# Performance work log

Hardware: AMD Instinct MI355X
Metric: run time of the kernel (lower is better)

Reference implementation:

```python
import jax, jax.numpy as jnp
import numpy as np

NUM_LAYERS = 2
D = 1024          # d_model
H = 16            # nhead
HD = D // H       # head_dim = 64
FF = 4096         # dim_feedforward
S, N, L = 1024, 2, 4096
EPS = 1e-5


def _layer_norm(x, g, b):
    mu = jnp.mean(x, axis=-1, keepdims=True)
    var = jnp.var(x, axis=-1, keepdims=True)
    return (x - mu) * jax.lax.rsqrt(var + EPS) * g + b


def setup_inputs() -> dict:
    key = jax.random.key(0)
    ks = jax.random.split(key, 16)
    w = 0.02
    return {
        "key_in": jax.random.normal(ks[0], (S, N, D), jnp.float32),
        "value_in": jax.random.normal(ks[1], (S, N, D), jnp.float32),
        "query": jax.random.normal(ks[2], (L, N, D), jnp.float32),
        "in_proj_w": jax.random.normal(ks[3], (NUM_LAYERS, 3 * D, D), jnp.float32) * w,
        "in_proj_b": jnp.zeros((NUM_LAYERS, 3 * D), jnp.float32),
        "out_w": jax.random.normal(ks[4], (NUM_LAYERS, D, D), jnp.float32) * w,
        "out_b": jnp.zeros((NUM_LAYERS, D), jnp.float32),
        "ln1_g": jnp.ones((NUM_LAYERS, D), jnp.float32),
        "ln1_b": jnp.zeros((NUM_LAYERS, D), jnp.float32),
        "ln2_g": jnp.ones((NUM_LAYERS, D), jnp.float32),
        "ln2_b": jnp.zeros((NUM_LAYERS, D), jnp.float32),
        "ff1_w": jax.random.normal(ks[5], (NUM_LAYERS, FF, D), jnp.float32) * w,
        "ff1_b": jnp.zeros((NUM_LAYERS, FF), jnp.float32),
        "ff2_w": jax.random.normal(ks[6], (NUM_LAYERS, D, FF), jnp.float32) * w,
        "ff2_b": jnp.zeros((NUM_LAYERS, D), jnp.float32),
    }


def reference(key_in, value_in, query, in_proj_w, in_proj_b, out_w, out_b,
              ln1_g, ln1_b, ln2_g, ln2_b, ff1_w, ff1_b, ff2_w, ff2_b):
    scaling = float(HD) ** -0.5
    noise_key = jax.random.key(42)
    tgt = query
    attn_map = None
    for i in range(NUM_LAYERS):
        Wq, Wk, Wv = in_proj_w[i, :D], in_proj_w[i, D:2 * D], in_proj_w[i, 2 * D:]
        bq, bk, bv = in_proj_b[i, :D], in_proj_b[i, D:2 * D], in_proj_b[i, 2 * D:]
        q = (tgt @ Wq.T + bq) * scaling              # [L,N,D]
        k = key_in @ Wk.T + bk                       # [S,N,D]
        v = value_in @ Wv.T + bv                     # [S,N,D]
        qh = q.reshape(L, N, H, HD).transpose(1, 2, 0, 3)   # [N,H,L,HD]
        kh = k.reshape(S, N, H, HD).transpose(1, 2, 0, 3)   # [N,H,S,HD]
        vh = v.reshape(S, N, H, HD).transpose(1, 2, 0, 3)   # [N,H,S,HD]
        scores = jnp.einsum('nhld,nhsd->nhls', qh, kh)      # [N,H,L,S]
        # add_noise_term: zero logit column + random value token
        scores = jnp.concatenate(
            [scores, jnp.zeros((N, H, L, 1), scores.dtype)], axis=-1)
        noise = jax.random.normal(jax.random.fold_in(noise_key, i),
                                  (N, H, 1, HD), vh.dtype)
        vh = jnp.concatenate([vh, noise], axis=2)           # [N,H,S+1,HD]
        w = jax.nn.softmax(scores, axis=-1)                 # [N,H,L,S+1]
        seg = jax.nn.sigmoid(w)                             # sigmoid of softmax
        out = jnp.einsum('nhls,nhsd->nhld', w, vh)          # [N,H,L,HD]
        out = out.transpose(2, 0, 1, 3).reshape(L, N, D)
        out = out @ out_w[i].T + out_b[i]
        attn_map = seg.mean(axis=1)[:, :, :-1]              # [N,L,S], noise col dropped
        x = _layer_norm(tgt + out, ln1_g[i], ln1_b[i])
        h = jax.nn.relu(x @ ff1_w[i].T + ff1_b[i]) @ ff2_w[i].T + ff2_b[i]
        tgt = _layer_norm(x + h, ln2_g[i], ln2_b[i])
    return tgt, attn_map
```

## Files before the change

### kernel.cpp

```cpp
#include <hip/hip_runtime.h>
#include <hip/hip_bf16.h>


typedef __bf16 bf16x8 __attribute__((ext_vector_type(8)));
typedef float  f32x4  __attribute__((ext_vector_type(4)));

__device__ __forceinline__ f32x4 mfma16(bf16x8 a, bf16x8 b, f32x4 c) {
    return __builtin_amdgcn_mfma_f32_16x16x32_bf16(a, b, c, 0, 0, 0);
}

__device__ __forceinline__ void load_lds16(const __bf16* g, __bf16* l) {
    __builtin_amdgcn_global_load_lds(
        (const __attribute__((address_space(1))) void*)g,
        (__attribute__((address_space(3))) void*)l, 16, 0, 0);
}

__device__ __forceinline__ int swz8(int o, int nwg) {
    return (o & 7) * (nwg >> 3) + (o >> 3);
}

__global__ __launch_bounds__(256) void cast_k(const float* __restrict__ in,
                                              __bf16* __restrict__ out, int n4) {
    int i = blockIdx.x * 256 + threadIdx.x;
    if (i >= n4) return;
    float4 f = ((const float4*)in)[i];
    union { uint2 u; __bf16 h[4]; } ob;
    ob.h[0] = (__bf16)f.x; ob.h[1] = (__bf16)f.y;
    ob.h[2] = (__bf16)f.z; ob.h[3] = (__bf16)f.w;
    ((uint2*)out)[i] = ob.u;
}

__global__ __launch_bounds__(512, 2) void gemm8p(
    const __bf16* __restrict__ A, const __bf16* __restrict__ B,
    const float* __restrict__ bias, __bf16* __restrict__ C,
    int Mt, int N, int K, float scale, int relu)
{
    __shared__ __bf16 L[8][8192];
    const int tid = threadIdx.x;
    const int wid = tid >> 6, lane = tid & 63;
    const int lq = lane >> 4, lc = lane & 15;
    const int wm = wid >> 2;
    const int wn = (wid & 3) * 64;
    const int bh = wn >> 7;
    const int lb = wn & 127;
    const int sw = lc & 7;
    const int w = swz8(blockIdx.x, gridDim.x);
    const int bm = (w % Mt) * 256, bn = (w / Mt) * 256;
    const int NT = K >> 6;

    auto stageA = [&](int kt, int h) {
#pragma unroll
        for (int p = 0; p < 2; ++p) {
            const int cc = p * 512 + tid;
            const int row = cc >> 3, gk = ((cc & 7) ^ (row & 7)) * 8;
            load_lds16(A + (size_t)(bm + h * 128 + row) * K + (kt * 64 + gk),
                       &L[(kt & 1) * 4 + h][(size_t)cc * 8]);
        }
    };
    auto stageB = [&](int kt, int h) {
#pragma unroll
        for (int p = 0; p < 2; ++p) {
            const int cc = p * 512 + tid;
            const int row = cc >> 3, gk = ((cc & 7) ^ (row & 7)) * 8;
            load_lds16(B + (size_t)(bn + h * 128 + row) * K + (kt * 64 + gk),
                       &L[(kt & 1) * 4 + 2 + h][(size_t)cc * 8]);
        }
    };

    stageA(0, 0); stageA(0, 1); stageB(0, 0); stageB(0, 1);
    stageA(1, 0); stageA(1, 1); stageB(1, 0); stageB(1, 1);
    asm volatile("s_waitcnt vmcnt(8)" ::: "memory");
    __builtin_amdgcn_s_barrier();
    __builtin_amdgcn_sched_barrier(0);

    const f32x4 fz = {0.f, 0.f, 0.f, 0.f};
    f32x4 acc[2][4][4];
#pragma unroll
    for (int rh = 0; rh < 2; ++rh)
#pragma unroll
        for (int i = 0; i < 4; ++i)
#pragma unroll
            for (int jj = 0; jj < 4; ++jj) acc[rh][i][jj] = fz;

    for (int t = 0; t < NT; ++t) {
        const __bf16* __restrict__ Ah = &L[(t & 1) * 4 + wm][0];
        const __bf16* __restrict__ Bh = &L[(t & 1) * 4 + 2 + bh][0];
        const int pf = (t + 2 < NT);
        bf16x8 a[2][4], b0[2][2], b1[2][2];

#pragma unroll
        for (int kk = 0; kk < 2; ++kk) {
            const int sl = ((kk * 4 + lq) ^ sw) * 8;
#pragma unroll
            for (int i = 0; i < 4; ++i)
                a[kk][i] = *(const bf16x8*)&Ah[(i * 16 + lc) * 64 + sl];
#pragma unroll
            for (int j = 0; j < 2; ++j)
                b0[kk][j] = *(const bf16x8*)&Bh[(lb + j * 16 + lc) * 64 + sl];
        }
        __builtin_amdgcn_s_barrier();
        asm volatile("s_waitcnt lgkmcnt(0)" ::: "memory");
        __builtin_amdgcn_sched_barrier(0);
        __builtin_amdgcn_s_setprio(1);
#pragma unroll
        for (int kk = 0; kk < 2; ++kk)
#pragma unroll
            for (int i = 0; i < 4; ++i)
#pragma unroll
                for (int j = 0; j < 2; ++j)
                    acc[0][i][j] = mfma16(a[kk][i], b0[kk][j], acc[0][i][j]);
        __builtin_amdgcn_s_setprio(0);
        __builtin_amdgcn_s_barrier();
        __builtin_amdgcn_sched_barrier(0);

#pragma unroll
        for (int kk = 0; kk < 2; ++kk) {
            const int sl = ((kk * 4 + lq) ^ sw) * 8;
#pragma unroll
            for (int j = 0; j < 2; ++j)
                b1[kk][j] = *(const bf16x8*)&Bh[(lb + 32 + j * 16 + lc) * 64 + sl];
        }
        __builtin_amdgcn_s_barrier();
        asm volatile("s_waitcnt lgkmcnt(0)" ::: "memory");
        __builtin_amdgcn_sched_barrier(0);
        __builtin_amdgcn_s_setprio(1);
#pragma unroll
        for (int kk = 0; kk < 2; ++kk)
#pragma unroll
            for (int i = 0; i < 4; ++i)
#pragma unroll
                for (int j = 0; j < 2; ++j)
                    acc[0][i][2 + j] = mfma16(a[kk][i], b1[kk][j], acc[0][i][2 + j]);
        __builtin_amdgcn_s_setprio(0);
        __builtin_amdgcn_s_barrier();
        __builtin_amdgcn_sched_barrier(0);

#pragma unroll
        for (int kk = 0; kk < 2; ++kk) {
            const int sl = ((kk * 4 + lq) ^ sw) * 8;
#pragma unroll
            for (int i = 0; i < 4; ++i)
                a[kk][i] = *(const bf16x8*)&Ah[(64 + i * 16 + lc) * 64 + sl];
        }
        if (pf) { stageB(t + 2, 0); stageB(t + 2, 1); }
        __builtin_amdgcn_s_barrier();
        asm volatile("s_waitcnt lgkmcnt(0)" ::: "memory");
        __builtin_amdgcn_sched_barrier(0);
        __builtin_amdgcn_s_setprio(1);
#pragma unroll
        for (int kk = 0; kk < 2; ++kk)
#pragma unroll
            for (int i = 0; i < 4; ++i)
#pragma unroll
                for (int j = 0; j < 2; ++j)
                    acc[1][i][j] = mfma16(a[kk][i], b0[kk][j], acc[1][i][j]);
        __builtin_amdgcn_s_setprio(0);
        __builtin_amdgcn_s_barrier();
        __builtin_amdgcn_sched_barrier(0);

        if (pf) { stageA(t + 2, 0); stageA(t + 2, 1); }
        __builtin_amdgcn_s_barrier();
        __builtin_amdgcn_sched_barrier(0);
        __builtin_amdgcn_s_setprio(1);
#pragma unroll
        for (int kk = 0; kk < 2; ++kk)
#pragma unroll
            for (int i = 0; i < 4; ++i)
#pragma unroll
                for (int j = 0; j < 2; ++j)
                    acc[1][i][2 + j] = mfma16(a[kk][i], b1[kk][j], acc[1][i][2 + j]);
        __builtin_amdgcn_s_setprio(0);
        if (pf) asm volatile("s_waitcnt vmcnt(8)" ::: "memory");
        else    asm volatile("s_waitcnt vmcnt(0)" ::: "memory");
        __builtin_amdgcn_s_barrier();
        __builtin_amdgcn_sched_barrier(0);
    }

    float bv[4];
#pragma unroll
    for (int q = 0; q < 4; ++q) bv[q] = bias[bn + wn + q * 16 + lc];
#pragma unroll
    for (int rh = 0; rh < 2; ++rh)
#pragma unroll
        for (int i = 0; i < 4; ++i)
#pragma unroll
            for (int r = 0; r < 4; ++r) {
                const int row = bm + wm * 128 + rh * 64 + i * 16 + lq * 4 + r;
                const size_t base = (size_t)row * N + bn + wn + lc;
#pragma unroll
                for (int ch = 0; ch < 2; ++ch)
#pragma unroll
                    for (int j = 0; j < 2; ++j) {
                        float v = (acc[rh][i][ch * 2 + j][r] + bv[ch * 2 + j]) * scale;
                        if (relu) v = fmaxf(v, 0.f);
                        C[base + ch * 32 + j * 16] = (__bf16)v;
                    }
            }
}

template <int BN>
__device__ __forceinline__ void gemm_core(
    const __bf16* __restrict__ A, const __bf16* __restrict__ B,
    const float* __restrict__ bias, __bf16* __restrict__ C,
    int M, int N, int K, float scale, int relu, int bm, int bn,
    __bf16* As, __bf16* Bs)
{
    const int tid = threadIdx.x;
    const int wave = tid >> 6, lane = tid & 63;
    const int lq = lane >> 4, lc = lane & 15;
    const int WN = BN / 2;
    const int JT = WN / 16;
    const int wm = (wave >> 1) * 64, wn = (wave & 1) * WN;

    const f32x4 fz = {0.f, 0.f, 0.f, 0.f};
    f32x4 acc[4][4];
#pragma unroll
    for (int i = 0; i < 4; ++i)
#pragma unroll
        for (int j = 0; j < JT; ++j) acc[i][j] = fz;

    const int sw = lc & 7;

    for (int k0 = 0; k0 < K; k0 += 64) {
        __syncthreads();
#pragma unroll
        for (int i = 0; i < 4; ++i) {
            const int c = tid + 256 * i;
            const int row = c >> 3, gk = ((c & 7) ^ (row & 7)) * 8;
            load_lds16(A + (size_t)(bm + row) * K + (k0 + gk),
                       As + (size_t)c * 8);
        }
#pragma unroll
        for (int i = 0; i < BN / 32; ++i) {
            const int c = tid + 256 * i;
            const int row = c >> 3, gk = ((c & 7) ^ (row & 7)) * 8;
            load_lds16(B + (size_t)(bn + row) * K + (k0 + gk),
                       Bs + (size_t)c * 8);
        }
        __syncthreads();
#pragma unroll
        for (int kk = 0; kk < 2; ++kk) {
            bf16x8 af[4], bw[4];
            const int slot = ((kk * 4 + lq) ^ sw) * 8;
#pragma unroll
            for (int i = 0; i < 4; ++i)
                af[i] = *(const bf16x8*)&As[(wm + i * 16 + lc) * 64 + slot];
#pragma unroll
            for (int j = 0; j < JT; ++j)
                bw[j] = *(const bf16x8*)&Bs[(wn + j * 16 + lc) * 64 + slot];
#pragma unroll
            for (int i = 0; i < 4; ++i)
#pragma unroll
                for (int j = 0; j < JT; ++j)
                    acc[i][j] = mfma16(af[i], bw[j], acc[i][j]);
        }
    }

#pragma unroll
    for (int j = 0; j < JT; ++j) {
        const int col = bn + wn + j * 16 + lc;
        const float bv = bias[col];
#pragma unroll
        for (int i = 0; i < 4; ++i) {
#pragma unroll
            for (int r = 0; r < 4; ++r) {
                float v = (acc[i][j][r] + bv) * scale;
                if (relu) v = fmaxf(v, 0.f);
                const int row = bm + wm + i * 16 + lq * 4 + r;
                C[(size_t)row * N + col] = (__bf16)v;
            }
        }
    }
}

__global__ __launch_bounds__(256) void gemm64(
    const __bf16* __restrict__ A, const __bf16* __restrict__ B,
    const float* __restrict__ bias, __bf16* __restrict__ C,
    int M, int N, int K, float scale, int relu)
{
    __shared__ __bf16 As[128 * 64];
    __shared__ __bf16 Bs[64 * 64];
    const int nwg = gridDim.x * gridDim.y;
    const int o = blockIdx.y * gridDim.x + blockIdx.x;
    const int w = swz8(o, nwg);
    const int bx = w % gridDim.x, by = w / gridDim.x;
    gemm_core<64>(A, B, bias, C, M, N, K, scale, relu,
                  by * 128, bx * 64, As, Bs);
}

__global__ __launch_bounds__(256) void gemm_qkv(
    const __bf16* __restrict__ TGT, const __bf16* __restrict__ KIN,
    const __bf16* __restrict__ VIN, const __bf16* __restrict__ W,
    const float* __restrict__ bias, __bf16* __restrict__ PROJ,
    __bf16* __restrict__ KB, __bf16* __restrict__ VB)
{
    __shared__ __bf16 As[128 * 64];
    __shared__ __bf16 Bs[64 * 64];
    const int bid = swz8(blockIdx.x, 1536);
    const __bf16* A; __bf16* Cout; int M, t, seg; float scale;
    if (bid < 1024)      { seg = 0; t = bid;        A = TGT; Cout = PROJ; M = 8192; scale = 0.125f; }
    else if (bid < 1280) { seg = 1; t = bid - 1024; A = KIN; Cout = KB;   M = 2048; scale = 1.f; }
    else                 { seg = 2; t = bid - 1280; A = VIN; Cout = VB;   M = 2048; scale = 1.f; }
    gemm_core<64>(A, W + (size_t)seg * 1048576, bias + seg * 1024, Cout,
                  M, 1024, 1024, scale, 0, (t >> 4) * 128, (t & 15) * 64, As, Bs);
}

__global__ __launch_bounds__(256) void transpose_v(const __bf16* __restrict__ v,
                                                   __bf16* __restrict__ vt) {
    __shared__ __bf16 t[64][72];
    const int tid = threadIdx.x;
    const int s0 = blockIdx.x * 64, h = blockIdx.y, n = blockIdx.z;
#pragma unroll
    for (int i = 0; i < 2; ++i) {
        const int cc = tid + 256 * i, row = cc >> 3, kc = (cc & 7) * 8;
        *(uint4*)&t[row][kc] =
            *(const uint4*)(v + ((size_t)((s0 + row) * 2 + n)) * 1024 + h * 64 + kc);
    }
    __syncthreads();
#pragma unroll
    for (int i = 0; i < 2; ++i) {
        const int cc = tid + 256 * i, d = cc >> 3, jc = (cc & 7) * 8;
        __attribute__((aligned(16))) __bf16 tmp[8];
#pragma unroll
        for (int u = 0; u < 8; ++u) tmp[u] = t[jc + u][d];
        *(uint4*)(vt + ((size_t)((n * 16 + h) * 64 + d)) * 1024 + s0 + jc) = *(uint4*)tmp;
    }
}

__global__ __launch_bounds__(256) void attn_fused(
    const __bf16* __restrict__ q, const __bf16* __restrict__ kk,
    const __bf16* __restrict__ vt, float* __restrict__ cvec,
    __bf16* __restrict__ aout)
{
    __shared__ __bf16 qs[64][72];
    __shared__ __bf16 ks[64][72];
    __shared__ __bf16 vs[64][72];
    __shared__ __bf16 es[64][72];
    const int tid = threadIdx.x, wave = tid >> 6, lane = tid & 63;
    const int lq = lane >> 4, lc = lane & 15;
    const int o = (blockIdx.z * 16 + blockIdx.y) * 64 + blockIdx.x;
    const int w = swz8(o, 2048);
    const int l0 = (w & 63) * 64, h = (w >> 6) & 15, n = w >> 10;
    const int wr = wave * 16;
#pragma unroll
    for (int i = 0; i < 2; ++i) {
        const int cc = tid + 256 * i, row = cc >> 3, kc = (cc & 7) * 8;
        *(uint4*)&qs[row][kc] =
            *(const uint4*)(q + ((size_t)((l0 + row) * 2 + n)) * 1024 + h * 64 + kc);
    }
    const f32x4 fz = {0.f, 0.f, 0.f, 0.f};
    f32x4 oacc[4];
#pragma unroll
    for (int dj = 0; dj < 4; ++dj) oacc[dj] = fz;
    float den[4] = {0.f, 0.f, 0.f, 0.f};

    for (int st = 0; st < 16; ++st) {
        __syncthreads();
#pragma unroll
        for (int i = 0; i < 2; ++i) {
            const int cc = tid + 256 * i, row = cc >> 3, kc = (cc & 7) * 8;
            *(uint4*)&ks[row][kc] =
                *(const uint4*)(kk + ((size_t)((st * 64 + row) * 2 + n)) * 1024 + h * 64 + kc);
            *(uint4*)&vs[row][kc] =
                *(const uint4*)(vt + ((size_t)((n * 16 + h) * 64 + row)) * 1024 + st * 64 + kc);
        }
        __syncthreads();
        const bf16x8 a0 = *(const bf16x8*)&qs[wr + lc][lq * 8];
        const bf16x8 a1 = *(const bf16x8*)&qs[wr + lc][32 + lq * 8];
#pragma unroll
        for (int sj = 0; sj < 4; ++sj) {
            f32x4 acc = fz;
            const bf16x8 b0 = *(const bf16x8*)&ks[sj * 16 + lc][lq * 8];
            const bf16x8 b1 = *(const bf16x8*)&ks[sj * 16 + lc][32 + lq * 8];
            acc = mfma16(a0, b0, acc);
            acc = mfma16(a1, b1, acc);
#pragma unroll
            for (int r = 0; r < 4; ++r) {
                const float e = __expf(acc[r]);
                den[r] += e;
                es[wr + lq * 4 + r][sj * 16 + lc] = (__bf16)e;
            }
        }
        const bf16x8 w0 = *(const bf16x8*)&es[wr + lc][lq * 8];
        const bf16x8 w1 = *(const bf16x8*)&es[wr + lc][32 + lq * 8];
#pragma unroll
        for (int dj = 0; dj < 4; ++dj) {
            const bf16x8 v0 = *(const bf16x8*)&vs[dj * 16 + lc][lq * 8];
            const bf16x8 v1 = *(const bf16x8*)&vs[dj * 16 + lc][32 + lq * 8];
            oacc[dj] = mfma16(w0, v0, oacc[dj]);
            oacc[dj] = mfma16(w1, v1, oacc[dj]);
        }
    }
#pragma unroll
    for (int m = 1; m < 16; m <<= 1)
#pragma unroll
        for (int r = 0; r < 4; ++r) den[r] += __shfl_xor(den[r], m);
    float c_r[4];
#pragma unroll
    for (int r = 0; r < 4; ++r) c_r[r] = 1.f / (den[r] + 1.f);
    if (lc == 0) {
#pragma unroll
        for (int r = 0; r < 4; ++r)
            cvec[((size_t)(n * 16 + h)) * 4096 + (l0 + wr + lq * 4 + r)] = c_r[r];
    }
#pragma unroll
    for (int r = 0; r < 4; ++r) {
        const int l = l0 + wr + lq * 4 + r;
        const size_t base = ((size_t)l * 2 + n) * 1024 + h * 64 + lc;
#pragma unroll
        for (int dj = 0; dj < 4; ++dj)
            aout[base + dj * 16] = (__bf16)(oacc[dj][r] * c_r[r]);
    }
}

__global__ __launch_bounds__(256) void attn_map_k(
    const __bf16* __restrict__ q, const __bf16* __restrict__ kk,
    const float* __restrict__ cvec, float* __restrict__ amap)
{
    __shared__ __bf16 qs[64][72];
    __shared__ __bf16 ks[64][72];
    const int tid = threadIdx.x, wave = tid >> 6, lane = tid & 63;
    const int lq = lane >> 4, lc = lane & 15;
    const int o = (blockIdx.z * 16 + blockIdx.y) * 64 + blockIdx.x;
    const int w = swz8(o, 2048);
    const int l0 = (w & 63) * 64, st = (w >> 6) & 15, n = w >> 10;
    const int wr = wave * 16;
    float sig[4][4];
#pragma unroll
    for (int sj = 0; sj < 4; ++sj)
#pragma unroll
        for (int r = 0; r < 4; ++r) sig[sj][r] = 0.f;

    for (int h = 0; h < 16; ++h) {
        __syncthreads();
#pragma unroll
        for (int i = 0; i < 2; ++i) {
            const int cc = tid + 256 * i, row = cc >> 3, kc = (cc & 7) * 8;
            *(uint4*)&qs[row][kc] =
                *(const uint4*)(q + ((size_t)((l0 + row) * 2 + n)) * 1024 + h * 64 + kc);
            *(uint4*)&ks[row][kc] =
                *(const uint4*)(kk + ((size_t)((st * 64 + row) * 2 + n)) * 1024 + h * 64 + kc);
        }
        __syncthreads();
        float c_r[4];
#pragma unroll
        for (int r = 0; r < 4; ++r)
            c_r[r] = cvec[((size_t)(n * 16 + h)) * 4096 + (l0 + wr + lq * 4 + r)];
        const bf16x8 a0 = *(const bf16x8*)&qs[wr + lc][lq * 8];
        const bf16x8 a1 = *(const bf16x8*)&qs[wr + lc][32 + lq * 8];
#pragma unroll
        for (int sj = 0; sj < 4; ++sj) {
            const f32x4 fz = {0.f, 0.f, 0.f, 0.f};
            f32x4 acc = fz;
            const bf16x8 b0 = *(const bf16x8*)&ks[sj * 16 + lc][lq * 8];
            const bf16x8 b1 = *(const bf16x8*)&ks[sj * 16 + lc][32 + lq * 8];
            acc = mfma16(a0, b0, acc);
            acc = mfma16(a1, b1, acc);
#pragma unroll
            for (int r = 0; r < 4; ++r) {
                const float ww = __expf(acc[r]) * c_r[r];
                const float w2 = ww * ww;
                sig[sj][r] += 0.5f + ww * (0.25f - w2 * (1.f / 48.f - w2 * (1.f / 480.f)));
            }
        }
    }
#pragma unroll
    for (int r = 0; r < 4; ++r) {
        const int l = l0 + wr + lq * 4 + r;
        const size_t base = ((size_t)n * 4096 + l) * 1024 + st * 64 + lc;
#pragma unroll
        for (int sj = 0; sj < 4; ++sj)
            amap[base + sj * 16] = sig[sj][r] * (1.f / 16.f);
    }
}

__global__ __launch_bounds__(256) void ln_k(
    const float* __restrict__ basef, const __bf16* __restrict__ baseb,
    const __bf16* __restrict__ add,
    const float* __restrict__ g, const float* __restrict__ bb,
    float* __restrict__ out_f32, __bf16* __restrict__ out_bf)
{
    __shared__ float red[8];
    const int row = blockIdx.x, tid = threadIdx.x;
    const int col = tid * 4;
    const size_t off = (size_t)row * 1024 + col;
    float v[4];
    if (basef) {
        float4 t = *(const float4*)(basef + off);
        v[0] = t.x; v[1] = t.y; v[2] = t.z; v[3] = t.w;
    } else {
        union { uint2 u; __bf16 h[4]; } tb;
        tb.u = *(const uint2*)(baseb + off);
#pragma unroll
        for (int j = 0; j < 4; ++j) v[j] = (float)tb.h[j];
    }
    {
        union { uint2 u; __bf16 h[4]; } ub;
        ub.u = *(const uint2*)(add + off);
#pragma unroll
        for (int j = 0; j < 4; ++j) v[j] += (float)ub.h[j];
    }
    float s = v[0] + v[1] + v[2] + v[3];
    float q = v[0] * v[0] + v[1] * v[1] + v[2] * v[2] + v[3] * v[3];
#pragma unroll
    for (int m = 1; m < 64; m <<= 1) { s += __shfl_xor(s, m); q += __shfl_xor(q, m); }
    const int wave = tid >> 6, lane = tid & 63;
    if (lane == 0) { red[wave] = s; red[4 + wave] = q; }
    __syncthreads();
    s = red[0] + red[1] + red[2] + red[3];
    q = red[4] + red[5] + red[6] + red[7];
    const float mu = s * (1.f / 1024.f);
    const float var = q * (1.f / 1024.f) - mu * mu;
    const float rs = rsqrtf(var + 1e-5f);
    const float4 gv = *(const float4*)(g + col);
    const float4 bv = *(const float4*)(bb + col);
    float y[4];
    y[0] = (v[0] - mu) * rs * gv.x + bv.x;
    y[1] = (v[1] - mu) * rs * gv.y + bv.y;
    y[2] = (v[2] - mu) * rs * gv.z + bv.z;
    y[3] = (v[3] - mu) * rs * gv.w + bv.w;
    if (out_f32) {
        float4 o; o.x = y[0]; o.y = y[1]; o.z = y[2]; o.w = y[3];
        *(float4*)(out_f32 + off) = o;
    }
    if (out_bf) {
        union { uint2 u; __bf16 h[4]; } ob;
#pragma unroll
        for (int j = 0; j < 4; ++j) ob.h[j] = (__bf16)y[j];
        *(uint2*)(out_bf + off) = ob.u;
    }
}

extern "C" void kernel_launch(void* const* d_in, const int* in_sizes, int n_in,
                              void* d_out, int out_size, void* d_ws, size_t ws_size,
                              hipStream_t stream) {
    const float* key_in    = (const float*)d_in[0];
    const float* value_in  = (const float*)d_in[1];
    const float* query     = (const float*)d_in[2];
    const float* in_proj_w = (const float*)d_in[3];
    const float* in_proj_b = (const float*)d_in[4];
    const float* out_w     = (const float*)d_in[5];
    const float* out_b     = (const float*)d_in[6];
    const float* ln1_g     = (const float*)d_in[7];
    const float* ln1_b     = (const float*)d_in[8];
    const float* ln2_g     = (const float*)d_in[9];
    const float* ln2_b     = (const float*)d_in[10];
    const float* ff1_w     = (const float*)d_in[11];
    const float* ff1_b     = (const float*)d_in[12];
    const float* ff2_w     = (const float*)d_in[13];
    const float* ff2_b     = (const float*)d_in[14];
    float* outp = (float*)d_out;

    __bf16* ws = (__bf16*)d_ws;
    const size_t M1 = 1048576;
    __bf16* WQKV = ws;
    __bf16* WOUT = ws + 6 * M1;
    __bf16* WF1  = ws + 8 * M1;
    __bf16* WF2  = ws + 16 * M1;
    __bf16* KIN  = ws + 24 * M1;
    __bf16* VIN  = ws + 26 * M1;
    __bf16* TGT  = ws + 28 * M1;
    __bf16* PROJ = ws + 36 * M1;
    __bf16* KB   = ws + 44 * M1;
    __bf16* VB   = ws + 46 * M1;
    __bf16* VT   = ws + 48 * M1;
    __bf16* AOUT = ws + 50 * M1;
    __bf16* XB   = ws + 58 * M1;
    __bf16* H1   = ws + 66 * M1;
    float*  CVEC = (float*)(ws + 98 * M1);

    cast_k<<<8192, 256, 0, stream>>>(query, TGT, 2097152);
    cast_k<<<2048, 256, 0, stream>>>(key_in, KIN, 524288);
    cast_k<<<2048, 256, 0, stream>>>(value_in, VIN, 524288);
    cast_k<<<6144, 256, 0, stream>>>(in_proj_w, WQKV, 1572864);
    cast_k<<<2048, 256, 0, stream>>>(out_w, WOUT, 524288);
    cast_k<<<8192, 256, 0, stream>>>(ff1_w, WF1, 2097152);
    cast_k<<<8192, 256, 0, stream>>>(ff2_w, WF2, 2097152);

    for (int i = 0; i < 2; ++i) {
        __bf16* WQKVi = WQKV + (size_t)i * 3 * M1;
        __bf16* WOUTi = WOUT + (size_t)i * M1;
        __bf16* WF1i  = WF1 + (size_t)i * 4 * M1;
        __bf16* WF2i  = WF2 + (size_t)i * 4 * M1;

        gemm_qkv<<<1536, 256, 0, stream>>>(TGT, KIN, VIN, WQKVi,
                                           in_proj_b + i * 3072, PROJ, KB, VB);
        transpose_v<<<dim3(16, 16, 2), 256, 0, stream>>>(VB, VT);

        attn_fused<<<dim3(64, 16, 2), 256, 0, stream>>>(PROJ, KB, VT, CVEC, AOUT);
        if (i == 1)
            attn_map_k<<<dim3(64, 16, 2), 256, 0, stream>>>(PROJ, KB, CVEC,
                                                            outp + 8388608);

        gemm64<<<dim3(16, 64), 256, 0, stream>>>(AOUT, WOUTi, out_b + i * 1024,
                                                 PROJ, 8192, 1024, 1024, 1.f, 0);
        ln_k<<<8192, 256, 0, stream>>>(i == 0 ? query : nullptr,
                                       i == 0 ? nullptr : TGT,
                                       PROJ, ln1_g + i * 1024, ln1_b + i * 1024,
                                       nullptr, XB);
        gemm8p<<<512, 512, 0, stream>>>(XB, WF1i, ff1_b + i * 4096,
                                        H1, 32, 4096, 1024, 1.f, 1);
        gemm64<<<dim3(16, 64), 256, 0, stream>>>(H1, WF2i, ff2_b + i * 1024,
                                                 AOUT, 8192, 1024, 4096, 1.f, 0);
        ln_k<<<8192, 256, 0, stream>>>(nullptr, XB, AOUT,
                                       ln2_g + i * 1024, ln2_b + i * 1024,
                                       i == 1 ? outp : nullptr, TGT);
    }
}
```

Measured before the change: 936.4 us.

## Replace 128x64 GEMM with 256x128 double-buffered 8-wave kernel for N=1024 GEMMs

Adds gemm8pN, a 512-thread kernel with 256x128 tiles, XOR-swizzled LDS staged through global_load_lds, two-stage prefetch and MFMA priority hints. It replaces the older gemm64 kernel for the out-projection and FF2 GEMMs (N=1024). The larger tile raises data reuse and cuts global traffic per flop, but the grid drops to 256 workgroups on a device with 256 CUs, so there is only about one wave of work. The LDS footprint is large.

```diff
diff --git a/kernel.cpp b/kernel.cpp
--- a/kernel.cpp
+++ b/kernel.cpp
@@ -198,6 +198,125 @@
             }
 }
 
+__global__ __launch_bounds__(512, 2) void gemm8pN(
+    const __bf16* __restrict__ A, const __bf16* __restrict__ B,
+    const float* __restrict__ bias, __bf16* __restrict__ C,
+    int Mt, int N, int K, float scale, int relu)
+{
+    __shared__ __bf16 L[6][8192];
+    const int tid = threadIdx.x;
+    const int wid = tid >> 6, lane = tid & 63;
+    const int lq = lane >> 4, lc = lane & 15;
+    const int wha = wid >> 2;
+    const int wn = (wid & 3) * 32;
+    const int sw = lc & 7;
+    const int w = swz8(blockIdx.x, gridDim.x);
+    const int bm = (w % Mt) * 256, bn = (w / Mt) * 128;
+    const int NT = K >> 6;
+
+    auto stageA = [&](int kt, int h) {
+#pragma unroll
+        for (int p = 0; p < 2; ++p) {
+            const int cc = p * 512 + tid;
+            const int row = cc >> 3, gk = ((cc & 7) ^ (row & 7)) * 8;
+            load_lds16(A + (size_t)(bm + h * 128 + row) * K + (kt * 64 + gk),
+                       &L[(kt & 1) * 3 + h][(size_t)cc * 8]);
+        }
+    };
+    auto stageB = [&](int kt) {
+#pragma unroll
+        for (int p = 0; p < 2; ++p) {
+            const int cc = p * 512 + tid;
+            const int row = cc >> 3, gk = ((cc & 7) ^ (row & 7)) * 8;
+            load_lds16(B + (size_t)(bn + row) * K + (kt * 64 + gk),
+                       &L[(kt & 1) * 3 + 2][(size_t)cc * 8]);
+        }
+    };
+
+    stageA(0, 0); stageA(0, 1); stageB(0);
+    stageA(1, 0); stageA(1, 1); stageB(1);
+    asm volatile("s_waitcnt vmcnt(6)" ::: "memory");
+    __builtin_amdgcn_s_barrier();
+    __builtin_amdgcn_sched_barrier(0);
+
+    const f32x4 fz = {0.f, 0.f, 0.f, 0.f};
+    f32x4 acc[2][4][2];
+#pragma unroll
+    for (int rh = 0; rh < 2; ++rh)
+#pragma unroll
+        for (int i = 0; i < 4; ++i)
+#pragma unroll
+            for (int j = 0; j < 2; ++j) acc[rh][i][j] = fz;
+
+    for (int t = 0; t < NT; ++t) {
+        const __bf16* __restrict__ Ah = &L[(t & 1) * 3 + wha][0];
+        const __bf16* __restrict__ Bb = &L[(t & 1) * 3 + 2][0];
+        const int pf = (t + 2 < NT);
+        bf16x8 a0[2][4], a1[2][4], b[2][2];
+
+#pragma unroll
+        for (int kk = 0; kk < 2; ++kk) {
+            const int sl = ((kk * 4 + lq) ^ sw) * 8;
+#pragma unroll
+            for (int i = 0; i < 4; ++i) {
+                a0[kk][i] = *(const bf16x8*)&Ah[(i * 16 + lc) * 64 + sl];
+                a1[kk][i] = *(const bf16x8*)&Ah[(64 + i * 16 + lc) * 64 + sl];
+            }
+#pragma unroll
+            for (int j = 0; j < 2; ++j)
+                b[kk][j] = *(const bf16x8*)&Bb[(wn + j * 16 + lc) * 64 + sl];
+        }
+        __builtin_amdgcn_s_barrier();
+        asm volatile("s_waitcnt lgkmcnt(0)" ::: "memory");
+        __builtin_amdgcn_sched_barrier(0);
+        __builtin_amdgcn_s_setprio(1);
+#pragma unroll
+        for (int kk = 0; kk < 2; ++kk)
+#pragma unroll
+            for (int i = 0; i < 4; ++i)
+#pragma unroll
+                for (int j = 0; j < 2; ++j)
+                    acc[0][i][j] = mfma16(a0[kk][i], b[kk][j], acc[0][i][j]);
+        __builtin_amdgcn_s_setprio(0);
+        __builtin_amdgcn_s_barrier();
+        __builtin_amdgcn_sched_barrier(0);
+
+        if (pf) { stageB(t + 2); stageA(t + 2, 0); stageA(t + 2, 1); }
+        __builtin_amdgcn_s_setprio(1);
+#pragma unroll
+        for (int kk = 0; kk < 2; ++kk)
+#pragma unroll
+            for (int i = 0; i < 4; ++i)
+#pragma unroll
+                for (int j = 0; j < 2; ++j)
+                    acc[1][i][j] = mfma16(a1[kk][i], b[kk][j], acc[1][i][j]);
+        __builtin_amdgcn_s_setprio(0);
+        if (pf) asm volatile("s_waitcnt vmcnt(6)" ::: "memory");
+        else    asm volatile("s_waitcnt vmcnt(0)" ::: "memory");
+        __builtin_amdgcn_s_barrier();
+        __builtin_amdgcn_sched_barrier(0);
+    }
+
+    float bv[2];
+    bv[0] = bias[bn + wn + lc];
+    bv[1] = bias[bn + wn + 16 + lc];
+#pragma unroll
+    for (int rh = 0; rh < 2; ++rh)
+#pragma unroll
+        for (int i = 0; i < 4; ++i)
+#pragma unroll
+            for (int r = 0; r < 4; ++r) {
+                const int row = bm + wha * 128 + rh * 64 + i * 16 + lq * 4 + r;
+                const size_t base = (size_t)row * N + bn + wn + lc;
+#pragma unroll
+                for (int j = 0; j < 2; ++j) {
+                    float v = (acc[rh][i][j][r] + bv[j]) * scale;
+                    if (relu) v = fmaxf(v, 0.f);
+                    C[base + j * 16] = (__bf16)v;
+                }
+            }
+}
+
 template <int BN>
 __device__ __forceinline__ void gemm_core(
     const __bf16* __restrict__ A, const __bf16* __restrict__ B,
@@ -271,21 +390,6 @@
             }
         }
     }
-}
-
-__global__ __launch_bounds__(256) void gemm64(
-    const __bf16* __restrict__ A, const __bf16* __restrict__ B,
-    const float* __restrict__ bias, __bf16* __restrict__ C,
-    int M, int N, int K, float scale, int relu)
-{
-    __shared__ __bf16 As[128 * 64];
-    __shared__ __bf16 Bs[64 * 64];
-    const int nwg = gridDim.x * gridDim.y;
-    const int o = blockIdx.y * gridDim.x + blockIdx.x;
-    const int w = swz8(o, nwg);
-    const int bx = w % gridDim.x, by = w / gridDim.x;
-    gemm_core<64>(A, B, bias, C, M, N, K, scale, relu,
-                  by * 128, bx * 64, As, Bs);
 }
 
 __global__ __launch_bounds__(256) void gemm_qkv(
@@ -592,16 +696,16 @@
             attn_map_k<<<dim3(64, 16, 2), 256, 0, stream>>>(PROJ, KB, CVEC,
                                                             outp + 8388608);
 
-        gemm64<<<dim3(16, 64), 256, 0, stream>>>(AOUT, WOUTi, out_b + i * 1024,
-                                                 PROJ, 8192, 1024, 1024, 1.f, 0);
+        gemm8pN<<<256, 512, 0, stream>>>(AOUT, WOUTi, out_b + i * 1024,
+                                         PROJ, 32, 1024, 1024, 1.f, 0);
         ln_k<<<8192, 256, 0, stream>>>(i == 0 ? query : nullptr,
                                        i == 0 ? nullptr : TGT,
                                        PROJ, ln1_g + i * 1024, ln1_b + i * 1024,
                                        nullptr, XB);
         gemm8p<<<512, 512, 0, stream>>>(XB, WF1i, ff1_b + i * 4096,
                                         H1, 32, 4096, 1024, 1.f, 1);
-        gemm64<<<dim3(16, 64), 256, 0, stream>>>(H1, WF2i, ff2_b + i * 1024,
-                                                 AOUT, 8192, 1024, 4096, 1.f, 0);
+        gemm8pN<<<256, 512, 0, stream>>>(H1, WF2i, ff2_b + i * 1024,
+                                         AOUT, 32, 1024, 4096, 1.f, 0);
         ln_k<<<8192, 256, 0, stream>>>(nullptr, XB, AOUT,
                                        ln2_g + i * 1024, ln2_b + i * 1024,
                                        i == 1 ? outp : nullptr, TGT);
```

Result: faster. 914.8 us (-2.3%).
